# Kernel tuning notes

Measured on AMD Instinct MI355X. Metric: run time of the kernel, lower is better.

## Reference

```python
import jax, jax.numpy as jnp
import numpy as np

N_NODES = 50000
N_EDGES = 25000
NNZ = 800000
IN_DIM = 256
OUT_DIM = 256


def setup_inputs() -> dict:
    key = jax.random.key(0)
    k1, k2, k3, k4, k5 = jax.random.split(key, 5)
    X = jax.random.normal(k1, (N_NODES, IN_DIM), dtype=jnp.float32)
    node_idx = jax.random.randint(k2, (NNZ,), 0, N_NODES, dtype=jnp.int64)
    edge_idx = jax.random.randint(k3, (NNZ,), 0, N_EDGES, dtype=jnp.int64)
    # Xavier-uniform-ish weight, zero bias (matches reset_parameters)
    limit = float(np.sqrt(6.0 / (IN_DIM + OUT_DIM)))
    W = jax.random.uniform(k4, (IN_DIM, OUT_DIM), dtype=jnp.float32, minval=-limit, maxval=limit)
    b = jnp.zeros((OUT_DIM,), dtype=jnp.float32)
    return {"X": X, "node_idx": node_idx, "edge_idx": edge_idx, "W": W, "b": b}


def reference(X, node_idx, edge_idx, W, b):
    # Y = X @ W + b  -- dense GEMM
    Y = X @ W + b  # [N, out_dim]

    ones = jnp.ones(node_idx.shape[0], dtype=Y.dtype)
    # D_v = rowsum(H)^-0.5 (inf -> 0); D_e = colsum(H)^-1 (inf -> 0)
    deg_v = jax.ops.segment_sum(ones, node_idx, num_segments=N_NODES)
    deg_e = jax.ops.segment_sum(ones, edge_idx, num_segments=N_EDGES)
    d_v = jnp.where(deg_v > 0, deg_v ** -0.5, 0.0)  # [N]
    d_e = jnp.where(deg_e > 0, 1.0 / deg_e, 0.0)    # [E]

    # step1 = H^T @ (D_v X): gather scaled node rows, scatter-add into edges
    Z = d_v[:, None] * Y                                   # [N, out_dim]
    step1 = jax.ops.segment_sum(Z[node_idx], edge_idx, num_segments=N_EDGES)  # [E, out_dim]
    # step2 = D_e @ step1
    step2 = d_e[:, None] * step1                           # [E, out_dim]
    # step3 = H @ step2: gather edge rows, scatter-add into nodes
    step3 = jax.ops.segment_sum(step2[edge_idx], node_idx, num_segments=N_NODES)  # [N, out_dim]
    # final = D_v @ step3
    return d_v[:, None] * step3
```

## Files before the change

kernel.cpp:

```cpp
#include <hip/hip_runtime.h>

#define N_NODES 50000
#define N_EDGES 25000
#define NNZ     800000
#define DIM     256

#define CAP_E 88
#define CAP_V 56

#define NBE 98
#define NBV 196
#define CE_COARSE 8800
#define CV_COARSE 4500
#define NNZ_PB 2048
#define P1_BLOCKS 391

#define B_A1   0
#define B_CE   0
#define B_CV   3449600
#define B_CSRE 12800000
#define B_CSRV 17200000
#define B_WT   22800000
#define B_CURV 22931072
#define B_CURE 23131072
#define B_S1B  23231072
#define B_CCUR 23331072
#define B_DV   23332248

typedef __attribute__((ext_vector_type(8))) short s8v;
typedef __attribute__((ext_vector_type(4))) float f4v;

__device__ __forceinline__ unsigned short f2bf(float f) {
    unsigned u = __float_as_uint(f);
    u = (u + 0x7FFFu + ((u >> 16) & 1u)) >> 16;
    return (unsigned short)u;
}
__device__ __forceinline__ float bf2f(unsigned short h) {
    return __uint_as_float(((unsigned)h) << 16);
}

__global__ __launch_bounds__(256) void k_prep(
        const float* __restrict__ X, const float* __restrict__ W,
        const int* __restrict__ node_idx, const int* __restrict__ edge_idx,
        unsigned short* __restrict__ Xb, unsigned short* __restrict__ WTb,
        unsigned* __restrict__ ccurE, unsigned* __restrict__ ccurV,
        unsigned* __restrict__ coarseE, unsigned* __restrict__ coarseV) {
    if (blockIdx.x < 6250) {
        size_t i = ((size_t)blockIdx.x * 256 + threadIdx.x) * 8;
        float4 p0 = *(const float4*)(X + i);
        float4 p1 = *(const float4*)(X + i + 4);
        unsigned short o[8] = {f2bf(p0.x), f2bf(p0.y), f2bf(p0.z), f2bf(p0.w),
                               f2bf(p1.x), f2bf(p1.y), f2bf(p1.z), f2bf(p1.w)};
        *(s8v*)(Xb + i) = *(const s8v*)o;
        return;
    }
    if (blockIdx.x < 6282) {
        int t = (blockIdx.x - 6250) * 256 + threadIdx.x;
        int n = t >> 5;
        int k0 = (t & 31) * 8;
        unsigned short o[8];
#pragma unroll
        for (int j = 0; j < 8; ++j) o[j] = f2bf(W[(size_t)(k0 + j) * DIM + n]);
        *(s8v*)(WTb + (size_t)n * DIM + k0) = *(const s8v*)o;
        return;
    }

    __shared__ unsigned histE[NBE], histV[NBV], baseE[NBE], baseV[NBV];
    __shared__ unsigned offE[NBE], offV[NBV];
    __shared__ unsigned nEs, nVs;
    __shared__ unsigned bufE[NNZ_PB], dstE[NNZ_PB];
    __shared__ unsigned bufV[NNZ_PB], dstV[NNZ_PB];
    const int tid = threadIdx.x;
    const int pb  = blockIdx.x - 6282;
    const int base = pb * NNZ_PB;

    if (tid < NBE) histE[tid] = 0;
    if (tid < NBV) histV[tid] = 0;
    __syncthreads();

    int idx0 = base + tid * 4;
    int idx1 = base + 1024 + tid * 4;
    bool ok0 = idx0 < NNZ, ok1 = idx1 < NNZ;
    int4 v0 = ok0 ? *(const int4*)(node_idx + idx0) : (int4){0,0,0,0};
    int4 e0 = ok0 ? *(const int4*)(edge_idx + idx0) : (int4){0,0,0,0};
    int4 v1 = ok1 ? *(const int4*)(node_idx + idx1) : (int4){0,0,0,0};
    int4 e1 = ok1 ? *(const int4*)(edge_idx + idx1) : (int4){0,0,0,0};
    int vv[8] = {v0.x, v0.y, v0.z, v0.w, v1.x, v1.y, v1.z, v1.w};
    int ee[8] = {e0.x, e0.y, e0.z, e0.w, e1.x, e1.y, e1.z, e1.w};

    unsigned short locE[8], locV[8];
#pragma unroll
    for (int j = 0; j < 8; ++j) {
        bool ok = (j < 4) ? ok0 : ok1;
        if (ok) {
            locE[j] = (unsigned short)atomicAdd(&histE[ee[j] >> 8], 1u);
            locV[j] = (unsigned short)atomicAdd(&histV[vv[j] >> 8], 1u);
        }
    }
    __syncthreads();
    if (tid < NBE) baseE[tid] = atomicAdd(&ccurE[tid], histE[tid]);
    if (tid < NBV) baseV[tid] = atomicAdd(&ccurV[tid], histV[tid]);
    if (tid == 0) { unsigned r = 0; for (int b = 0; b < NBE; ++b) { offE[b] = r; r += histE[b]; } nEs = r; }
    if (tid == 1) { unsigned r = 0; for (int b = 0; b < NBV; ++b) { offV[b] = r; r += histV[b]; } nVs = r; }
    __syncthreads();

#pragma unroll
    for (int j = 0; j < 8; ++j) {
        bool ok = (j < 4) ? ok0 : ok1;
        if (ok) {
            unsigned e = (unsigned)ee[j], v = (unsigned)vv[j];
            unsigned be = e >> 8, bv = v >> 8;
            unsigned se = offE[be] + locE[j];
            unsigned pe = baseE[be] + locE[j];
            bufE[se] = ((e & 255u) << 16) | v;
            dstE[se] = (pe < CE_COARSE) ? (be * CE_COARSE + pe) : 0xFFFFFFFFu;
            unsigned sv = offV[bv] + locV[j];
            unsigned pv = baseV[bv] + locV[j];
            bufV[sv] = ((v & 255u) << 16) | e;
            dstV[sv] = (pv < CV_COARSE) ? (bv * CV_COARSE + pv) : 0xFFFFFFFFu;
        }
    }
    __syncthreads();

    unsigned nE = nEs, nV = nVs;
    for (unsigned i = tid; i < nE; i += 256) {
        unsigned d = dstE[i];
        if (d != 0xFFFFFFFFu) coarseE[d] = bufE[i];
    }
    for (unsigned i = tid; i < nV; i += 256) {
        unsigned d = dstV[i];
        if (d != 0xFFFFFFFFu) coarseV[d] = bufV[i];
    }
}

__global__ __launch_bounds__(1024) void k_fine(
        const unsigned* __restrict__ coarseE, const unsigned* __restrict__ coarseV,
        const unsigned* __restrict__ ccurE, const unsigned* __restrict__ ccurV,
        unsigned short* __restrict__ csrE, unsigned short* __restrict__ csrV,
        unsigned* __restrict__ cur_e, unsigned* __restrict__ cur_v,
        float* __restrict__ dv) {
    __shared__ unsigned cnt[256];
    __shared__ unsigned short slots[256 * CAP_E];
    const int tid = threadIdx.x;
    if (tid < 256) cnt[tid] = 0;
    __syncthreads();

    if (blockIdx.x < NBE) {
        int b = blockIdx.x;
        unsigned n = ccurE[b]; n = n < CE_COARSE ? n : CE_COARSE;
        const unsigned* src = coarseE + (size_t)b * CE_COARSE;
        for (unsigned i = tid; i < n; i += 1024) {
            unsigned p = src[i];
            unsigned f = p >> 16, v = p & 0xFFFFu;
            unsigned pos = atomicAdd(&cnt[f], 1u);
            if (pos < CAP_E) slots[f * CAP_E + pos] = (unsigned short)v;
        }
        __syncthreads();
        if (tid < 256) {
            int e = b * 256 + tid;
            if (e < N_EDGES) cur_e[e] = cnt[tid];
        }
        int rows = N_EDGES - b * 256; rows = rows < 256 ? rows : 256;
        unsigned words = (unsigned)rows * (CAP_E / 2);
        unsigned* dst = (unsigned*)(csrE + (size_t)b * 256 * CAP_E);
        const unsigned* s = (const unsigned*)slots;
        for (unsigned i = tid; i < words; i += 1024) dst[i] = s[i];
    } else {
        int b = blockIdx.x - NBE;
        unsigned n = ccurV[b]; n = n < CV_COARSE ? n : CV_COARSE;
        const unsigned* src = coarseV + (size_t)b * CV_COARSE;
        for (unsigned i = tid; i < n; i += 1024) {
            unsigned p = src[i];
            unsigned f = p >> 16, e = p & 0xFFFFu;
            unsigned pos = atomicAdd(&cnt[f], 1u);
            if (pos < CAP_V) slots[f * CAP_V + pos] = (unsigned short)e;
        }
        __syncthreads();
        if (tid < 256) {
            int v = b * 256 + tid;
            if (v < N_NODES) {
                unsigned c = cnt[tid];
                cur_v[v] = c;
                dv[v] = c ? __frsqrt_rn((float)c) : 0.0f;
            }
        }
        int rows = N_NODES - b * 256; rows = rows < 256 ? rows : 256;
        unsigned words = (unsigned)rows * (CAP_V / 2);
        unsigned* dst = (unsigned*)(csrV + (size_t)b * 256 * CAP_V);
        const unsigned* s = (const unsigned*)slots;
        for (unsigned i = tid; i < words; i += 1024) dst[i] = s[i];
    }
}

__global__ __launch_bounds__(256) void k_gather_edges(
        const unsigned short* __restrict__ Xb,
        const unsigned short* __restrict__ csrE,
        const unsigned* __restrict__ cur_e,
        const float* __restrict__ dv,
        unsigned short* __restrict__ A1, float* __restrict__ s1b) {
    int w = (blockIdx.x * 256 + threadIdx.x) >> 6;
    int lane = threadIdx.x & 63;
    if (w >= N_EDGES) return;
    unsigned cnt = cur_e[w]; cnt = cnt < CAP_E ? cnt : CAP_E;
    const unsigned short* lst = csrE + (size_t)w * CAP_E;
    unsigned idp = (lane < CAP_E / 2) ? ((const unsigned*)lst)[lane] : 0u;
    const unsigned short* xb = Xb + (size_t)lane * 4;

    float ax = 0.f, ay = 0.f, az = 0.f, aw = 0.f, ss = 0.f;

#define EFETCH(J, X0, X1, X2, X3, S0, S1, S2, S3)                          \
    {                                                                      \
        unsigned p0 = __shfl(idp, (int)((J) >> 1));                        \
        unsigned p1 = __shfl(idp, (int)((J) >> 1) + 1);                    \
        unsigned v0 = p0 & 0xFFFFu, v1 = p0 >> 16;                         \
        unsigned v2 = p1 & 0xFFFFu, v3 = p1 >> 16;                         \
        S0 = dv[v0]; S1 = dv[v1]; S2 = dv[v2]; S3 = dv[v3];                \
        X0 = *(const ushort4*)(xb + ((size_t)v0 << 8));                    \
        X1 = *(const ushort4*)(xb + ((size_t)v1 << 8));                    \
        X2 = *(const ushort4*)(xb + ((size_t)v2 << 8));                    \
        X3 = *(const ushort4*)(xb + ((size_t)v3 << 8));                    \
    }
#define ECONS(X0, X1, X2, X3, S0, S1, S2, S3)                              \
    {                                                                      \
        ax = fmaf(S0, bf2f(X0.x), ax); ay = fmaf(S0, bf2f(X0.y), ay);      \
        az = fmaf(S0, bf2f(X0.z), az); aw = fmaf(S0, bf2f(X0.w), aw);      \
        ax = fmaf(S1, bf2f(X1.x), ax); ay = fmaf(S1, bf2f(X1.y), ay);      \
        az = fmaf(S1, bf2f(X1.z), az); aw = fmaf(S1, bf2f(X1.w), aw);      \
        ax = fmaf(S2, bf2f(X2.x), ax); ay = fmaf(S2, bf2f(X2.y), ay);      \
        az = fmaf(S2, bf2f(X2.z), az); aw = fmaf(S2, bf2f(X2.w), aw);      \
        ax = fmaf(S3, bf2f(X3.x), ax); ay = fmaf(S3, bf2f(X3.y), ay);      \
        az = fmaf(S3, bf2f(X3.z), az); aw = fmaf(S3, bf2f(X3.w), aw);      \
        ss += (S0 + S1) + (S2 + S3);                                       \
    }

    unsigned quads = cnt >> 2;
    unsigned j = 0;
    if (quads) {
        ushort4 a0, a1, a2, a3, b0, b1, b2, b3;
        float r0, r1, r2, r3, t0, t1, t2, t3;
        EFETCH(0u, a0, a1, a2, a3, r0, r1, r2, r3);
        unsigned q = 1;
        for (; q + 1 < quads; q += 2) {
            EFETCH(4u * q,      b0, b1, b2, b3, t0, t1, t2, t3);
            ECONS(a0, a1, a2, a3, r0, r1, r2, r3);
            EFETCH(4u * q + 4u, a0, a1, a2, a3, r0, r1, r2, r3);
            ECONS(b0, b1, b2, b3, t0, t1, t2, t3);
        }
        if (q < quads) {
            EFETCH(4u * q, b0, b1, b2, b3, t0, t1, t2, t3);
            ECONS(a0, a1, a2, a3, r0, r1, r2, r3);
            ECONS(b0, b1, b2, b3, t0, t1, t2, t3);
        } else {
            ECONS(a0, a1, a2, a3, r0, r1, r2, r3);
        }
        j = quads << 2;
    }
    for (; j < cnt; ++j) {
        unsigned p = __shfl(idp, (int)(j >> 1));
        unsigned v = (j & 1) ? (p >> 16) : (p & 0xFFFFu);
        float s = dv[v];
        ushort4 x = *(const ushort4*)(xb + ((size_t)v << 8));
        ax = fmaf(s, bf2f(x.x), ax); ay = fmaf(s, bf2f(x.y), ay);
        az = fmaf(s, bf2f(x.z), az); aw = fmaf(s, bf2f(x.w), aw);
        ss += s;
    }
#undef EFETCH
#undef ECONS

    ushort4 o = {f2bf(ax), f2bf(ay), f2bf(az), f2bf(aw)};
    *(ushort4*)(A1 + (size_t)w * DIM + lane * 4) = o;
    if (lane == 0) s1b[w] = ss;
}

__global__ __launch_bounds__(256) void k_gemm_mfma(
        const unsigned short* __restrict__ A,
        const unsigned short* __restrict__ WT,
        const float* __restrict__ bias,
        const unsigned* __restrict__ cur_e,
        const float* __restrict__ s1b,
        unsigned short* __restrict__ S2) {
    const int tid  = threadIdx.x;
    const int wv   = tid >> 6;
    const int lane = tid & 63;
    const int quad = lane >> 4;
    const int l16  = lane & 15;
    const int r0   = blockIdx.x * 64;
    const int nb   = wv * 64;

    f4v acc[4][4];
#pragma unroll
    for (int mt = 0; mt < 4; ++mt)
#pragma unroll
        for (int nt = 0; nt < 4; ++nt) acc[mt][nt] = (f4v){0.f, 0.f, 0.f, 0.f};

    for (int k0 = 0; k0 < DIM; k0 += 32) {
        s8v a[4], b[4];
#pragma unroll
        for (int nt = 0; nt < 4; ++nt) {
            int n = nb + nt * 16 + l16;
            b[nt] = *(const s8v*)(WT + (size_t)n * DIM + k0 + quad * 8);
        }
#pragma unroll
        for (int mt = 0; mt < 4; ++mt) {
            int m = r0 + mt * 16 + l16;
            m = (m < N_EDGES) ? m : (N_EDGES - 1);
            a[mt] = *(const s8v*)(A + (size_t)m * DIM + k0 + quad * 8);
        }
#pragma unroll
        for (int mt = 0; mt < 4; ++mt)
#pragma unroll
            for (int nt = 0; nt < 4; ++nt)
                acc[mt][nt] = __builtin_amdgcn_mfma_f32_16x16x32_bf16(
                    a[mt], b[nt], acc[mt][nt], 0, 0, 0);
    }

    __syncthreads();

    float bv[4];
#pragma unroll
    for (int nt = 0; nt < 4; ++nt) bv[nt] = bias[nb + nt * 16 + l16];

#pragma unroll
    for (int mt = 0; mt < 4; ++mt) {
#pragma unroll
        for (int reg = 0; reg < 4; ++reg) {
            int row = r0 + mt * 16 + quad * 4 + reg;
            if (row < N_EDGES) {
                unsigned ce = cur_e[row];
                float sc = ce ? 1.0f / (float)ce : 0.0f;
                float sb = s1b[row];
#pragma unroll
                for (int nt = 0; nt < 4; ++nt) {
                    float v = sc * (acc[mt][nt][reg] + sb * bv[nt]);
                    S2[(size_t)row * DIM + nb + nt * 16 + l16] = f2bf(v);
                }
            }
        }
    }
}

__global__ __launch_bounds__(256) void k_gather_nodes(
        const unsigned short* __restrict__ S2,
        const unsigned short* __restrict__ csrV,
        const unsigned* __restrict__ cur_v,
        const float* __restrict__ dv,
        float* __restrict__ out) {
    int w = (blockIdx.x * 256 + threadIdx.x) >> 6;
    int lane = threadIdx.x & 63;
    if (w >= N_NODES) return;
    unsigned cnt = cur_v[w]; cnt = cnt < CAP_V ? cnt : CAP_V;
    const unsigned short* lst = csrV + (size_t)w * CAP_V;
    unsigned idp = (lane < CAP_V / 2) ? ((const unsigned*)lst)[lane] : 0u;
    const unsigned short* sb = S2 + (size_t)lane * 4;

    float ax = 0.f, ay = 0.f, az = 0.f, aw = 0.f;

#define NFETCH(J, X0, X1, X2, X3)                                          \
    {                                                                      \
        unsigned p0 = __shfl(idp, (int)((J) >> 1));                        \
        unsigned p1 = __shfl(idp, (int)((J) >> 1) + 1);                    \
        unsigned e0 = p0 & 0xFFFFu, e1 = p0 >> 16;                         \
        unsigned e2 = p1 & 0xFFFFu, e3 = p1 >> 16;                         \
        X0 = *(const ushort4*)(sb + ((size_t)e0 << 8));                    \
        X1 = *(const ushort4*)(sb + ((size_t)e1 << 8));                    \
        X2 = *(const ushort4*)(sb + ((size_t)e2 << 8));                    \
        X3 = *(const ushort4*)(sb + ((size_t)e3 << 8));                    \
    }
#define NCONS(X0, X1, X2, X3)                                              \
    {                                                                      \
        ax += (bf2f(X0.x) + bf2f(X1.x)) + (bf2f(X2.x) + bf2f(X3.x));       \
        ay += (bf2f(X0.y) + bf2f(X1.y)) + (bf2f(X2.y) + bf2f(X3.y));       \
        az += (bf2f(X0.z) + bf2f(X1.z)) + (bf2f(X2.z) + bf2f(X3.z));       \
        aw += (bf2f(X0.w) + bf2f(X1.w)) + (bf2f(X2.w) + bf2f(X3.w));       \
    }

    unsigned quads = cnt >> 2;
    unsigned j = 0;
    if (quads) {
        ushort4 a0, a1, a2, a3, b0, b1, b2, b3;
        NFETCH(0u, a0, a1, a2, a3);
        unsigned q = 1;
        for (; q + 1 < quads; q += 2) {
            NFETCH(4u * q,      b0, b1, b2, b3);
            NCONS(a0, a1, a2, a3);
            NFETCH(4u * q + 4u, a0, a1, a2, a3);
            NCONS(b0, b1, b2, b3);
        }
        if (q < quads) {
            NFETCH(4u * q, b0, b1, b2, b3);
            NCONS(a0, a1, a2, a3);
            NCONS(b0, b1, b2, b3);
        } else {
            NCONS(a0, a1, a2, a3);
        }
        j = quads << 2;
    }
    for (; j < cnt; ++j) {
        unsigned p = __shfl(idp, (int)(j >> 1));
        unsigned e = (j & 1) ? (p >> 16) : (p & 0xFFFFu);
        ushort4 x = *(const ushort4*)(sb + ((size_t)e << 8));
        ax += bf2f(x.x); ay += bf2f(x.y); az += bf2f(x.z); aw += bf2f(x.w);
    }
#undef NFETCH
#undef NCONS

    float s = dv[w];
    float4 o = {s * ax, s * ay, s * az, s * aw};
    *(float4*)(out + (size_t)w * DIM + lane * 4) = o;
}

extern "C" void kernel_launch(void* const* d_in, const int* in_sizes, int n_in,
                              void* d_out, int out_size, void* d_ws, size_t ws_size,
                              hipStream_t stream) {
    (void)in_sizes; (void)n_in; (void)out_size; (void)ws_size;
    const float* X        = (const float*)d_in[0];
    const int*   node_idx = (const int*)d_in[1];
    const int*   edge_idx = (const int*)d_in[2];
    const float* W        = (const float*)d_in[3];
    const float* bias     = (const float*)d_in[4];
    float* out = (float*)d_out;
    char*  ws  = (char*)d_ws;

    unsigned short* A1      = (unsigned short*)(ws + B_A1);
    unsigned*       coarseE = (unsigned*)(ws + B_CE);
    unsigned*       coarseV = (unsigned*)(ws + B_CV);
    unsigned short* csrE    = (unsigned short*)(ws + B_CSRE);
    unsigned short* csrV    = (unsigned short*)(ws + B_CSRV);
    unsigned short* WTb     = (unsigned short*)(ws + B_WT);
    unsigned*       cur_v   = (unsigned*)(ws + B_CURV);
    unsigned*       cur_e   = (unsigned*)(ws + B_CURE);
    float*          s1b     = (float*)(ws + B_S1B);
    unsigned*       ccurE   = (unsigned*)(ws + B_CCUR);
    unsigned*       ccurV   = ccurE + NBE;
    float*          dv      = (float*)(ws + B_DV);

    unsigned short* Xb = (unsigned short*)d_out;

    (void)hipMemsetAsync(ccurE, 0, (NBE + NBV) * sizeof(unsigned), stream);

    k_prep<<<6282 + P1_BLOCKS, 256, 0, stream>>>(X, W, node_idx, edge_idx,
                                                 Xb, WTb, ccurE, ccurV, coarseE, coarseV);
    k_fine<<<NBE + NBV, 1024, 0, stream>>>(coarseE, coarseV, ccurE, ccurV,
                                           csrE, csrV, cur_e, cur_v, dv);
    k_gather_edges<<<(N_EDGES * 64 + 255) / 256, 256, 0, stream>>>(
        Xb, csrE, cur_e, dv, A1, s1b);
    k_gemm_mfma<<<(N_EDGES + 63) / 64, 256, 0, stream>>>(A1, WTb, bias, cur_e, s1b, A1);
    k_gather_nodes<<<(N_NODES * 64 + 255) / 256, 256, 0, stream>>>(
        A1, csrV, cur_v, dv, out);
}
```

Before: 256.5 us.

## Compute Y = XW on nodes first, fusing bf16 conversion into the GEMM

The GEMM moves from after edge aggregation (25k edge rows) to before it (50k node rows), matching the reference order. The X-to-bf16 conversion pass is folded into the new GEMM's operand loads, and the edge gather now applies the 1/deg_e scale directly. This drops the separate conversion kernel, the s1b bias-sum side channel and the post-gather GEMM, at the cost of doing twice as many GEMM rows and reading fp32 X uncached inside the GEMM.

```diff
diff --git a/kernel.cpp b/kernel.cpp
--- a/kernel.cpp
+++ b/kernel.cpp
@@ -23,7 +23,6 @@
 #define B_WT   22800000
 #define B_CURV 22931072
 #define B_CURE 23131072
-#define B_S1B  23231072
 #define B_CCUR 23331072
 #define B_DV   23332248
 
@@ -40,22 +39,13 @@
 }
 
 __global__ __launch_bounds__(256) void k_prep(
-        const float* __restrict__ X, const float* __restrict__ W,
+        const float* __restrict__ W,
         const int* __restrict__ node_idx, const int* __restrict__ edge_idx,
-        unsigned short* __restrict__ Xb, unsigned short* __restrict__ WTb,
+        unsigned short* __restrict__ WTb,
         unsigned* __restrict__ ccurE, unsigned* __restrict__ ccurV,
         unsigned* __restrict__ coarseE, unsigned* __restrict__ coarseV) {
-    if (blockIdx.x < 6250) {
-        size_t i = ((size_t)blockIdx.x * 256 + threadIdx.x) * 8;
-        float4 p0 = *(const float4*)(X + i);
-        float4 p1 = *(const float4*)(X + i + 4);
-        unsigned short o[8] = {f2bf(p0.x), f2bf(p0.y), f2bf(p0.z), f2bf(p0.w),
-                               f2bf(p1.x), f2bf(p1.y), f2bf(p1.z), f2bf(p1.w)};
-        *(s8v*)(Xb + i) = *(const s8v*)o;
-        return;
-    }
-    if (blockIdx.x < 6282) {
-        int t = (blockIdx.x - 6250) * 256 + threadIdx.x;
+    if (blockIdx.x < 32) {
+        int t = blockIdx.x * 256 + threadIdx.x;
         int n = t >> 5;
         int k0 = (t & 31) * 8;
         unsigned short o[8];
@@ -71,7 +61,7 @@
     __shared__ unsigned bufE[NNZ_PB], dstE[NNZ_PB];
     __shared__ unsigned bufV[NNZ_PB], dstV[NNZ_PB];
     const int tid = threadIdx.x;
-    const int pb  = blockIdx.x - 6282;
+    const int pb  = blockIdx.x - 32;
     const int base = pb * NNZ_PB;
 
     if (tid < NBE) histE[tid] = 0;
@@ -192,45 +182,111 @@
     }
 }
 
+__global__ __launch_bounds__(256) void k_gemm_y(
+        const float* __restrict__ X,
+        const unsigned short* __restrict__ WT,
+        const float* __restrict__ bias,
+        unsigned short* __restrict__ Yb) {
+    const int tid  = threadIdx.x;
+    const int wv   = tid >> 6;
+    const int lane = tid & 63;
+    const int quad = lane >> 4;
+    const int l16  = lane & 15;
+    const int r0   = blockIdx.x * 64;
+    const int nb   = wv * 64;
+
+    f4v acc[4][4];
+#pragma unroll
+    for (int mt = 0; mt < 4; ++mt)
+#pragma unroll
+        for (int nt = 0; nt < 4; ++nt) acc[mt][nt] = (f4v){0.f, 0.f, 0.f, 0.f};
+
+    for (int k0 = 0; k0 < DIM; k0 += 32) {
+        s8v a[4], b[4];
+#pragma unroll
+        for (int nt = 0; nt < 4; ++nt) {
+            int n = nb + nt * 16 + l16;
+            b[nt] = *(const s8v*)(WT + (size_t)n * DIM + k0 + quad * 8);
+        }
+#pragma unroll
+        for (int mt = 0; mt < 4; ++mt) {
+            int m = r0 + mt * 16 + l16;
+            m = (m < N_NODES) ? m : (N_NODES - 1);
+            const float* xp = X + (size_t)m * DIM + k0 + quad * 8;
+            float4 p0 = *(const float4*)xp;
+            float4 p1 = *(const float4*)(xp + 4);
+            unsigned short o[8] = {f2bf(p0.x), f2bf(p0.y), f2bf(p0.z), f2bf(p0.w),
+                                   f2bf(p1.x), f2bf(p1.y), f2bf(p1.z), f2bf(p1.w)};
+            a[mt] = *(const s8v*)o;
+        }
+#pragma unroll
+        for (int mt = 0; mt < 4; ++mt)
+#pragma unroll
+            for (int nt = 0; nt < 4; ++nt)
+                acc[mt][nt] = __builtin_amdgcn_mfma_f32_16x16x32_bf16(
+                    a[mt], b[nt], acc[mt][nt], 0, 0, 0);
+    }
+
+    float bv[4];
+#pragma unroll
+    for (int nt = 0; nt < 4; ++nt) bv[nt] = bias[nb + nt * 16 + l16];
+
+#pragma unroll
+    for (int mt = 0; mt < 4; ++mt) {
+#pragma unroll
+        for (int reg = 0; reg < 4; ++reg) {
+            int row = r0 + mt * 16 + quad * 4 + reg;
+            if (row < N_NODES) {
+#pragma unroll
+                for (int nt = 0; nt < 4; ++nt) {
+                    Yb[(size_t)row * DIM + nb + nt * 16 + l16] =
+                        f2bf(acc[mt][nt][reg] + bv[nt]);
+                }
+            }
+        }
+    }
+}
+
 __global__ __launch_bounds__(256) void k_gather_edges(
-        const unsigned short* __restrict__ Xb,
+        const unsigned short* __restrict__ Yb,
         const unsigned short* __restrict__ csrE,
         const unsigned* __restrict__ cur_e,
         const float* __restrict__ dv,
-        unsigned short* __restrict__ A1, float* __restrict__ s1b) {
+        unsigned short* __restrict__ S2) {
     int w = (blockIdx.x * 256 + threadIdx.x) >> 6;
     int lane = threadIdx.x & 63;
     if (w >= N_EDGES) return;
-    unsigned cnt = cur_e[w]; cnt = cnt < CAP_E ? cnt : CAP_E;
+    unsigned deg = cur_e[w];
+    unsigned cnt = deg < CAP_E ? deg : CAP_E;
+    float sc = deg ? 1.0f / (float)deg : 0.0f;
     const unsigned short* lst = csrE + (size_t)w * CAP_E;
     unsigned idp = (lane < CAP_E / 2) ? ((const unsigned*)lst)[lane] : 0u;
-    const unsigned short* xb = Xb + (size_t)lane * 4;
-
-    float ax = 0.f, ay = 0.f, az = 0.f, aw = 0.f, ss = 0.f;
-
-#define EFETCH(J, X0, X1, X2, X3, S0, S1, S2, S3)                          \
+    const unsigned short* xb = Yb + (size_t)lane * 4;
+
+    float ax = 0.f, ay = 0.f, az = 0.f, aw = 0.f;
+
+#define EFETCH(J, X0, X1, X2, X3, S0, S1, S2_, S3)                         \
     {                                                                      \
         unsigned p0 = __shfl(idp, (int)((J) >> 1));                        \
         unsigned p1 = __shfl(idp, (int)((J) >> 1) + 1);                    \
         unsigned v0 = p0 & 0xFFFFu, v1 = p0 >> 16;                         \
         unsigned v2 = p1 & 0xFFFFu, v3 = p1 >> 16;                         \
-        S0 = dv[v0]; S1 = dv[v1]; S2 = dv[v2]; S3 = dv[v3];                \
+        S0 = dv[v0]; S1 = dv[v1]; S2_ = dv[v2]; S3 = dv[v3];               \
         X0 = *(const ushort4*)(xb + ((size_t)v0 << 8));                    \
         X1 = *(const ushort4*)(xb + ((size_t)v1 << 8));                    \
         X2 = *(const ushort4*)(xb + ((size_t)v2 << 8));                    \
         X3 = *(const ushort4*)(xb + ((size_t)v3 << 8));                    \
     }
-#define ECONS(X0, X1, X2, X3, S0, S1, S2, S3)                              \
+#define ECONS(X0, X1, X2, X3, S0, S1, S2_, S3)                             \
     {                                                                      \
         ax = fmaf(S0, bf2f(X0.x), ax); ay = fmaf(S0, bf2f(X0.y), ay);      \
         az = fmaf(S0, bf2f(X0.z), az); aw = fmaf(S0, bf2f(X0.w), aw);      \
         ax = fmaf(S1, bf2f(X1.x), ax); ay = fmaf(S1, bf2f(X1.y), ay);      \
         az = fmaf(S1, bf2f(X1.z), az); aw = fmaf(S1, bf2f(X1.w), aw);      \
-        ax = fmaf(S2, bf2f(X2.x), ax); ay = fmaf(S2, bf2f(X2.y), ay);      \
-        az = fmaf(S2, bf2f(X2.z), az); aw = fmaf(S2, bf2f(X2.w), aw);      \
+        ax = fmaf(S2_, bf2f(X2.x), ax); ay = fmaf(S2_, bf2f(X2.y), ay);    \
+        az = fmaf(S2_, bf2f(X2.z), az); aw = fmaf(S2_, bf2f(X2.w), aw);    \
         ax = fmaf(S3, bf2f(X3.x), ax); ay = fmaf(S3, bf2f(X3.y), ay);      \
         az = fmaf(S3, bf2f(X3.z), az); aw = fmaf(S3, bf2f(X3.w), aw);      \
-        ss += (S0 + S1) + (S2 + S3);                                       \
     }
 
     unsigned quads = cnt >> 2;
@@ -262,81 +318,12 @@
         ushort4 x = *(const ushort4*)(xb + ((size_t)v << 8));
         ax = fmaf(s, bf2f(x.x), ax); ay = fmaf(s, bf2f(x.y), ay);
         az = fmaf(s, bf2f(x.z), az); aw = fmaf(s, bf2f(x.w), aw);
-        ss += s;
     }
 #undef EFETCH
 #undef ECONS
 
-    ushort4 o = {f2bf(ax), f2bf(ay), f2bf(az), f2bf(aw)};
-    *(ushort4*)(A1 + (size_t)w * DIM + lane * 4) = o;
-    if (lane == 0) s1b[w] = ss;
-}
-
-__global__ __launch_bounds__(256) void k_gemm_mfma(
-        const unsigned short* __restrict__ A,
-        const unsigned short* __restrict__ WT,
-        const float* __restrict__ bias,
-        const unsigned* __restrict__ cur_e,
-        const float* __restrict__ s1b,
-        unsigned short* __restrict__ S2) {
-    const int tid  = threadIdx.x;
-    const int wv   = tid >> 6;
-    const int lane = tid & 63;
-    const int quad = lane >> 4;
-    const int l16  = lane & 15;
-    const int r0   = blockIdx.x * 64;
-    const int nb   = wv * 64;
-
-    f4v acc[4][4];
-#pragma unroll
-    for (int mt = 0; mt < 4; ++mt)
-#pragma unroll
-        for (int nt = 0; nt < 4; ++nt) acc[mt][nt] = (f4v){0.f, 0.f, 0.f, 0.f};
-
-    for (int k0 = 0; k0 < DIM; k0 += 32) {
-        s8v a[4], b[4];
-#pragma unroll
-        for (int nt = 0; nt < 4; ++nt) {
-            int n = nb + nt * 16 + l16;
-            b[nt] = *(const s8v*)(WT + (size_t)n * DIM + k0 + quad * 8);
-        }
-#pragma unroll
-        for (int mt = 0; mt < 4; ++mt) {
-            int m = r0 + mt * 16 + l16;
-            m = (m < N_EDGES) ? m : (N_EDGES - 1);
-            a[mt] = *(const s8v*)(A + (size_t)m * DIM + k0 + quad * 8);
-        }
-#pragma unroll
-        for (int mt = 0; mt < 4; ++mt)
-#pragma unroll
-            for (int nt = 0; nt < 4; ++nt)
-                acc[mt][nt] = __builtin_amdgcn_mfma_f32_16x16x32_bf16(
-                    a[mt], b[nt], acc[mt][nt], 0, 0, 0);
-    }
-
-    __syncthreads();
-
-    float bv[4];
-#pragma unroll
-    for (int nt = 0; nt < 4; ++nt) bv[nt] = bias[nb + nt * 16 + l16];
-
-#pragma unroll
-    for (int mt = 0; mt < 4; ++mt) {
-#pragma unroll
-        for (int reg = 0; reg < 4; ++reg) {
-            int row = r0 + mt * 16 + quad * 4 + reg;
-            if (row < N_EDGES) {
-                unsigned ce = cur_e[row];
-                float sc = ce ? 1.0f / (float)ce : 0.0f;
-                float sb = s1b[row];
-#pragma unroll
-                for (int nt = 0; nt < 4; ++nt) {
-                    float v = sc * (acc[mt][nt][reg] + sb * bv[nt]);
-                    S2[(size_t)row * DIM + nb + nt * 16 + l16] = f2bf(v);
-                }
-            }
-        }
-    }
+    ushort4 o = {f2bf(sc * ax), f2bf(sc * ay), f2bf(sc * az), f2bf(sc * aw)};
+    *(ushort4*)(S2 + (size_t)w * DIM + lane * 4) = o;
 }
 
 __global__ __launch_bounds__(256) void k_gather_nodes(
@@ -421,7 +408,7 @@
     float* out = (float*)d_out;
     char*  ws  = (char*)d_ws;
 
-    unsigned short* A1      = (unsigned short*)(ws + B_A1);
+    unsigned short* S2      = (unsigned short*)(ws + B_A1);
     unsigned*       coarseE = (unsigned*)(ws + B_CE);
     unsigned*       coarseV = (unsigned*)(ws + B_CV);
     unsigned short* csrE    = (unsigned short*)(ws + B_CSRE);
@@ -429,22 +416,21 @@
     unsigned short* WTb     = (unsigned short*)(ws + B_WT);
     unsigned*       cur_v   = (unsigned*)(ws + B_CURV);
     unsigned*       cur_e   = (unsigned*)(ws + B_CURE);
-    float*          s1b     = (float*)(ws + B_S1B);
     unsigned*       ccurE   = (unsigned*)(ws + B_CCUR);
     unsigned*       ccurV   = ccurE + NBE;
     float*          dv      = (float*)(ws + B_DV);
 
-    unsigned short* Xb = (unsigned short*)d_out;
+    unsigned short* Yb = (unsigned short*)d_out;
 
     (void)hipMemsetAsync(ccurE, 0, (NBE + NBV) * sizeof(unsigned), stream);
 
-    k_prep<<<6282 + P1_BLOCKS, 256, 0, stream>>>(X, W, node_idx, edge_idx,
-                                                 Xb, WTb, ccurE, ccurV, coarseE, coarseV);
+    k_prep<<<32 + P1_BLOCKS, 256, 0, stream>>>(W, node_idx, edge_idx,
+                                               WTb, ccurE, ccurV, coarseE, coarseV);
     k_fine<<<NBE + NBV, 1024, 0, stream>>>(coarseE, coarseV, ccurE, ccurV,
                                            csrE, csrV, cur_e, cur_v, dv);
+    k_gemm_y<<<(N_NODES + 63) / 64, 256, 0, stream>>>(X, WTb, bias, Yb);
     k_gather_edges<<<(N_EDGES * 64 + 255) / 256, 256, 0, stream>>>(
-        Xb, csrE, cur_e, dv, A1, s1b);
-    k_gemm_mfma<<<(N_EDGES + 63) / 64, 256, 0, stream>>>(A1, WTb, bias, cur_e, s1b, A1);
+        Yb, csrE, cur_e, dv, S2);
     k_gather_nodes<<<(N_NODES * 64 + 255) / 256, 256, 0, stream>>>(
-        A1, csrV, cur_v, dv, out);
-}
+        S2, csrV, cur_v, dv, out);
+}
```

New measurement: 272.6 us. 1.06x slower.
